# Performance work log

Measured on AMD Instinct MI355X. Metric: run time of the kernel, lower is better.

## Reference

```python
import jax, jax.numpy as jnp
import numpy as np

N_EMBD = 1024
N_HEAD = 16
B, T = 2, 2048
EPS_LN = 1e-5
EPS_RENORM = 1e-8


def _layernorm(x, w, b):
    mu = jnp.mean(x, axis=-1, keepdims=True)
    var = jnp.mean(jnp.square(x - mu), axis=-1, keepdims=True)
    return (x - mu) * jax.lax.rsqrt(var + EPS_LN) * w + b


def setup_inputs() -> dict:
    key = jax.random.key(0)
    ks = jax.random.split(key, 8)
    C = N_EMBD
    s = 0.02
    return {
        "x": jax.random.normal(ks[0], (B, T, C), jnp.float32),
        "ln1_w": jnp.ones((C,), jnp.float32),
        "ln1_b": jnp.zeros((C,), jnp.float32),
        "w_attn": jax.random.normal(ks[1], (C, 3 * C), jnp.float32) * s,
        "b_attn": jnp.zeros((3 * C,), jnp.float32),
        "w_attn_proj": jax.random.normal(ks[2], (C, C), jnp.float32) * s,
        "b_attn_proj": jnp.zeros((C,), jnp.float32),
        "threshold": jnp.full((N_HEAD,), 0.01, jnp.float32),
        "leak": jnp.full((N_HEAD,), 2.0, jnp.float32),
        "steepness": jnp.full((N_HEAD,), 2.0, jnp.float32),
        "ln2_w": jnp.ones((C,), jnp.float32),
        "ln2_b": jnp.zeros((C,), jnp.float32),
        "w_fc": jax.random.normal(ks[3], (C, 4 * C), jnp.float32) * s,
        "b_fc": jnp.zeros((4 * C,), jnp.float32),
        "w_mlp_proj": jax.random.normal(ks[4], (4 * C, C), jnp.float32) * s,
        "b_mlp_proj": jnp.zeros((C,), jnp.float32),
    }


def _ember_block(x, ln1_w, ln1_b, w_attn, b_attn, w_attn_proj, b_attn_proj,
                 threshold, leak, steepness, ln2_w, ln2_b,
                 w_fc, b_fc, w_mlp_proj, b_mlp_proj):
    Bx, Tx, C = x.shape
    H = N_HEAD
    D = C // H

    h = _layernorm(x, ln1_w, ln1_b)
    qkv = h @ w_attn + b_attn                      # [B,T,3C]
    q, k, v = jnp.split(qkv, 3, axis=-1)
    q = q.reshape(Bx, Tx, H, D).transpose(0, 2, 1, 3)  # [B,H,T,D]
    k = k.reshape(Bx, Tx, H, D).transpose(0, 2, 1, 3)
    v = v.reshape(Bx, Tx, H, D).transpose(0, 2, 1, 3)

    att = jnp.einsum('bhqd,bhkd->bhqk', q, k) * (1.0 / np.sqrt(D))
    causal = jnp.tril(jnp.ones((Tx, Tx), bool))
    att = jnp.where(causal[None, None], att, -jnp.inf)
    p = jax.nn.softmax(att, axis=-1)               # [B,H,T,T]

    # per-head LIF gating
    th = (jnp.abs(threshold) * 0.1)[None, :, None, None]
    lk = jax.nn.sigmoid(leak)[None, :, None, None]
    st = jax.nn.softplus(steepness)[None, :, None, None]
    fire = jax.nn.sigmoid(st * (p - th))
    w = fire + lk * (1.0 - fire)
    m = p * w
    m = m / (jnp.sum(m, axis=-1, keepdims=True) + EPS_RENORM)

    y = jnp.einsum('bhqk,bhkd->bhqd', m, v)
    y = y.transpose(0, 2, 1, 3).reshape(Bx, Tx, C)
    y = y @ w_attn_proj + b_attn_proj
    x = x + y

    h2 = _layernorm(x, ln2_w, ln2_b)
    h2 = jax.nn.gelu(h2 @ w_fc + b_fc, approximate=False)
    x = x + (h2 @ w_mlp_proj + b_mlp_proj)
    return x


def reference(x, ln1_w, ln1_b, w_attn, b_attn, w_attn_proj, b_attn_proj,
              threshold, leak, steepness, ln2_w, ln2_b,
              w_fc, b_fc, w_mlp_proj, b_mlp_proj):
    return _ember_block(x, ln1_w, ln1_b, w_attn, b_attn, w_attn_proj, b_attn_proj,
                        threshold, leak, steepness, ln2_w, ln2_b,
                        w_fc, b_fc, w_mlp_proj, b_mlp_proj)
```

## Files before the change

### kernel.cpp

```cpp
#include <hip/hip_runtime.h>
#include <hip/hip_bf16.h>
#include <math.h>

typedef __bf16 bf16_t;
typedef __bf16 bf16x8 __attribute__((ext_vector_type(8)));
typedef __bf16 bf16x4 __attribute__((ext_vector_type(4)));
typedef float  f32x4  __attribute__((ext_vector_type(4)));
typedef unsigned int u32;

static constexpr int C_    = 1024;
static constexpr int NH    = 16;
static constexpr int DH    = 64;
static constexpr int BB    = 2;
static constexpr int TT    = 2048;
static constexpr int MROWS = BB * TT;
static constexpr float LOG2E = 1.4426950408889634f;

__device__ __forceinline__ void gload_lds16(const bf16_t* src, bf16_t* dst) {
  __builtin_amdgcn_global_load_lds(
      (const __attribute__((address_space(1))) u32*)(src),
      (__attribute__((address_space(3))) u32*)(dst),
      16, 0, 0);
}

__device__ __forceinline__ u32 cvt_pk_bf16(float a, float b) {
  u32 r;
  asm("v_cvt_pk_bf16_f32 %0, %1, %2" : "=v"(r) : "v"(a), "v"(b));
  return r;
}

__device__ __forceinline__ float fexp2(float x) {
#if __has_builtin(__builtin_amdgcn_exp2f)
  return __builtin_amdgcn_exp2f(x);
#else
  return exp2f(x);
#endif
}
__device__ __forceinline__ float frcp(float x) {
#if __has_builtin(__builtin_amdgcn_rcpf)
  return __builtin_amdgcn_rcpf(x);
#else
  return 1.0f / x;
#endif
}

__device__ __forceinline__ int sc_to_t(int s, int c) {
  if (s < 32)  return s;
  if (s < 64)  return 32 + (s - 32) * 2 + c;
  if (s < 96)  return 96 + (s - 64) * 3 + c;
  return 192 + (s - 96) * 4 + c;
}

__device__ __forceinline__ void item64_to_uc(int item, int& u, int& c) {
  if (item < 8)       { u = item;               c = 0; }
  else if (item < 24) { int v = item - 8;  u = 8  + (v >> 1); c = v & 1; }
  else if (item < 48) { int v = item - 24; u = 16 + v / 3;    c = v - 3 * (v / 3); }
  else                { int v = item - 48; u = 24 + (v >> 2); c = v & 3; }
}

__global__ __launch_bounds__(256) void ln_bf16(
    const float* __restrict__ x, const float* __restrict__ w,
    const float* __restrict__ b, bf16_t* __restrict__ out)
{
  const int row = blockIdx.x;
  const int tid = threadIdx.x;
  const float4 v = reinterpret_cast<const float4*>(x + (size_t)row * C_)[tid];
  float s  = v.x + v.y + v.z + v.w;
  float s2 = v.x*v.x + v.y*v.y + v.z*v.z + v.w*v.w;
#pragma unroll
  for (int m = 1; m < 64; m <<= 1) { s += __shfl_xor(s, m); s2 += __shfl_xor(s2, m); }
  __shared__ float red[8];
  const int wv = tid >> 6;
  if ((tid & 63) == 0) { red[wv] = s; red[4 + wv] = s2; }
  __syncthreads();
  s  = red[0] + red[1] + red[2] + red[3];
  s2 = red[4] + red[5] + red[6] + red[7];
  const float mu   = s * (1.0f / C_);
  const float rstd = rsqrtf(s2 * (1.0f / C_) - mu * mu + 1e-5f);
  const float4 wv4 = reinterpret_cast<const float4*>(w)[tid];
  const float4 bv4 = reinterpret_cast<const float4*>(b)[tid];
  bf16x4 o;
  o[0] = (bf16_t)((v.x - mu) * rstd * wv4.x + bv4.x);
  o[1] = (bf16_t)((v.y - mu) * rstd * wv4.y + bv4.y);
  o[2] = (bf16_t)((v.z - mu) * rstd * wv4.z + bv4.z);
  o[3] = (bf16_t)((v.w - mu) * rstd * wv4.w + bv4.w);
  *reinterpret_cast<bf16x4*>(out + (size_t)row * C_ + tid * 4) = o;
}

__global__ __launch_bounds__(256) void ln2_fuse(
    const float* __restrict__ p0, const bf16_t* __restrict__ p1,
    const float* __restrict__ xin, const float* __restrict__ pbias,
    const float* __restrict__ w, const float* __restrict__ b,
    float* __restrict__ x2out, bf16_t* __restrict__ out)
{
  const int row = blockIdx.x;
  const int tid = threadIdx.x;
  const size_t base = (size_t)row * C_ + tid * 4;
  const float4 v0 = *reinterpret_cast<const float4*>(p0 + base);
  const bf16x4 v1 = *reinterpret_cast<const bf16x4*>(p1 + base);
  const float4 xr = *reinterpret_cast<const float4*>(xin + base);
  const float4 pb = *reinterpret_cast<const float4*>(pbias + tid * 4);
  float4 v;
  v.x = v0.x + (float)v1[0] + pb.x + xr.x;
  v.y = v0.y + (float)v1[1] + pb.y + xr.y;
  v.z = v0.z + (float)v1[2] + pb.z + xr.z;
  v.w = v0.w + (float)v1[3] + pb.w + xr.w;
  *reinterpret_cast<float4*>(x2out + base) = v;

  float s  = v.x + v.y + v.z + v.w;
  float s2 = v.x*v.x + v.y*v.y + v.z*v.z + v.w*v.w;
#pragma unroll
  for (int m = 1; m < 64; m <<= 1) { s += __shfl_xor(s, m); s2 += __shfl_xor(s2, m); }
  __shared__ float red[8];
  const int wv = tid >> 6;
  if ((tid & 63) == 0) { red[wv] = s; red[4 + wv] = s2; }
  __syncthreads();
  s  = red[0] + red[1] + red[2] + red[3];
  s2 = red[4] + red[5] + red[6] + red[7];
  const float mu   = s * (1.0f / C_);
  const float rstd = rsqrtf(s2 * (1.0f / C_) - mu * mu + 1e-5f);
  const float4 wv4 = reinterpret_cast<const float4*>(w)[tid];
  const float4 bv4 = reinterpret_cast<const float4*>(b)[tid];
  bf16x4 o;
  o[0] = (bf16_t)((v.x - mu) * rstd * wv4.x + bv4.x);
  o[1] = (bf16_t)((v.y - mu) * rstd * wv4.y + bv4.y);
  o[2] = (bf16_t)((v.z - mu) * rstd * wv4.z + bv4.z);
  o[3] = (bf16_t)((v.w - mu) * rstd * wv4.w + bv4.w);
  *reinterpret_cast<bf16x4*>(out + base) = o;
}

__global__ __launch_bounds__(256) void combine3(
    float* __restrict__ out, const bf16_t* __restrict__ p1,
    const bf16_t* __restrict__ p2, const bf16_t* __restrict__ p3,
    const float* __restrict__ bias, const float* __restrict__ resid)
{
  const size_t idx = ((size_t)blockIdx.x * 256 + threadIdx.x) * 4;
  float4 o = *reinterpret_cast<const float4*>(out + idx);
  const bf16x4 a = *reinterpret_cast<const bf16x4*>(p1 + idx);
  const bf16x4 b = *reinterpret_cast<const bf16x4*>(p2 + idx);
  const bf16x4 c = *reinterpret_cast<const bf16x4*>(p3 + idx);
  const float4 r = *reinterpret_cast<const float4*>(resid + idx);
  const int col = (int)(idx & (C_ - 1));
  const float4 bv = *reinterpret_cast<const float4*>(bias + col);
  o.x += (float)a[0] + (float)b[0] + (float)c[0] + bv.x + r.x;
  o.y += (float)a[1] + (float)b[1] + (float)c[1] + bv.y + r.y;
  o.z += (float)a[2] + (float)b[2] + (float)c[2] + bv.z + r.z;
  o.w += (float)a[3] + (float)b[3] + (float)c[3] + bv.w + r.w;
  *reinterpret_cast<float4*>(out + idx) = o;
}

__global__ __launch_bounds__(256) void transpose_w(
    const float* __restrict__ in, bf16_t* __restrict__ out, int K, int N)
{
  __shared__ float tile[32][33];
  const int tx = threadIdx.x & 31, ty = threadIdx.x >> 5;
  const int n0 = blockIdx.x * 32, k0 = blockIdx.y * 32;
#pragma unroll
  for (int i = 0; i < 4; ++i)
    tile[ty + i * 8][tx] = in[(size_t)(k0 + ty + i * 8) * N + n0 + tx];
  __syncthreads();
#pragma unroll
  for (int i = 0; i < 4; ++i)
    out[(size_t)(n0 + ty + i * 8) * K + k0 + tx] = (bf16_t)tile[tx][ty + i * 8];
}

__global__ __launch_bounds__(256) void transpose_v(
    const bf16_t* __restrict__ in, bf16_t* __restrict__ out)
{
  __shared__ bf16_t tile[32][33];
  const int bh = blockIdx.z;
  const bf16_t* src = in  + (size_t)bh * TT * DH;
  bf16_t*       dst = out + (size_t)bh * TT * DH;
  const int tx = threadIdx.x & 31, ty = threadIdx.x >> 5;
  const int t0 = blockIdx.x * 32, d0 = blockIdx.y * 32;
#pragma unroll
  for (int i = 0; i < 4; ++i)
    tile[ty + i * 8][tx] = src[(size_t)(t0 + ty + i * 8) * DH + d0 + tx];
  __syncthreads();
#pragma unroll
  for (int i = 0; i < 4; ++i)
    dst[(size_t)(d0 + ty + i * 8) * TT + t0 + tx] = tile[tx][ty + i * 8];
}

template<int EPI>
__global__ __launch_bounds__(512, 2) void gemm256(
    const bf16_t* __restrict__ A, const bf16_t* __restrict__ Bt,
    const float* __restrict__ bias, bf16_t* __restrict__ bout0,
    bf16_t* __restrict__ bout1, bf16_t* __restrict__ bout2,
    int N, int K, int nbn)
{
  __shared__ bf16_t As[2][256 * 64];
  __shared__ bf16_t Bs[2][256 * 64];
  const int tid  = threadIdx.x;
  const int wave = tid >> 6, lane = tid & 63;
  const int r = lane & 15, g = lane >> 4;
  const int wm = wave >> 2, wn = wave & 3;

  const int cpx = gridDim.x >> 3;
  const int swz = (blockIdx.x & 7) * cpx + (blockIdx.x >> 3);
  const int bm = swz / nbn, bn = swz - bm * nbn;

  const bf16_t* Abase = A  + (size_t)bm * 256 * K;
  const bf16_t* Bbase = Bt + (size_t)bn * 256 * K;

  f32x4 acc[8][4] = {};

  auto STAGE = [&](int b, int kt) {
#pragma unroll
    for (int it = 0; it < 4; ++it) {
      const int idx = it * 512 + tid;
      const int rr = idx >> 3, cc = idx & 7, gs = cc ^ (rr & 7);
      gload_lds16(Abase + (size_t)rr * K + kt + gs * 8, &As[b][idx * 8]);
      gload_lds16(Bbase + (size_t)rr * K + kt + gs * 8, &Bs[b][idx * 8]);
    }
  };

  const int NT = K >> 6;
  STAGE(0, 0);
  for (int t = 0; t < NT; ++t) {
    const int b = t & 1;
    if (t + 1 < NT) {
      STAGE(b ^ 1, (t + 1) << 6);
      asm volatile("s_waitcnt vmcnt(8)" ::: "memory");
    } else {
      asm volatile("s_waitcnt vmcnt(0)" ::: "memory");
    }
    __builtin_amdgcn_s_barrier();
    asm volatile("" ::: "memory");
#pragma unroll
    for (int s2 = 0; s2 < 2; ++s2) {
      bf16x8 af[8], bfr[4];
#pragma unroll
      for (int mi = 0; mi < 8; ++mi) {
        const int rr = wm * 128 + mi * 16 + r;
        const int ch = (s2 * 4 + g) ^ (rr & 7);
        af[mi] = *reinterpret_cast<const bf16x8*>(&As[b][rr * 64 + ch * 8]);
      }
#pragma unroll
      for (int ni = 0; ni < 4; ++ni) {
        const int rr = wn * 64 + ni * 16 + r;
        const int ch = (s2 * 4 + g) ^ (rr & 7);
        bfr[ni] = *reinterpret_cast<const bf16x8*>(&Bs[b][rr * 64 + ch * 8]);
      }
      __builtin_amdgcn_s_setprio(1);
#pragma unroll
      for (int mi = 0; mi < 8; ++mi)
#pragma unroll
        for (int ni = 0; ni < 4; ++ni)
          acc[mi][ni] = __builtin_amdgcn_mfma_f32_16x16x32_bf16(
              af[mi], bfr[ni], acc[mi][ni], 0, 0, 0);
      __builtin_amdgcn_s_setprio(0);
    }
    asm volatile("" ::: "memory");
    __builtin_amdgcn_s_barrier();
  }

#pragma unroll
  for (int mi = 0; mi < 8; ++mi) {
#pragma unroll
    for (int ni = 0; ni < 4; ++ni) {
      const int grow0 = bm * 256 + wm * 128 + mi * 16 + g * 4;
      const int gcol  = bn * 256 + wn * 64 + ni * 16 + r;
      const float bv = bias[gcol];
#pragma unroll
      for (int i = 0; i < 4; ++i) {
        const int grow = grow0 + i;
        const float v = acc[mi][ni][i] + bv;
        if constexpr (EPI == 0) {
          const int which = gcol >> 10;
          const int c0 = gcol & 1023;
          const int hh = c0 >> 6, dd = c0 & 63;
          const int bb = grow >> 11, tt = grow & 2047;
          bf16_t* dst = (which == 0) ? bout0 : (which == 1) ? bout1 : bout2;
          dst[((size_t)(bb * NH + hh) * TT + tt) * DH + dd] = (bf16_t)v;
        } else {
          const float gl = 0.5f * v * (1.0f + erff(v * 0.70710678118654752f));
          bout0[(size_t)grow * N + gcol] = (bf16_t)gl;
        }
      }
    }
  }
}

template<int EPI>
__global__ __launch_bounds__(256) void gemm_bf16(
    const bf16_t* __restrict__ A, const bf16_t* __restrict__ Bt,
    const float* __restrict__ bias, const float* __restrict__ resid,
    float* __restrict__ fout, bf16_t* __restrict__ bout0,
    bf16_t* __restrict__ bout1, bf16_t* __restrict__ bout2,
    int M, int N, int Kc, int Kfull)
{
  constexpr int BM = 128, BN = 128, BK = 64;
  __shared__ bf16_t As[BM * BK];
  __shared__ bf16_t Bs[BN * BK];
  const int tid  = threadIdx.x;
  const int wave = tid >> 6, lane = tid & 63;
  const int r = lane & 15, g = lane >> 4;
  const int wm = wave >> 1, wn = wave & 1;
  const int bm = blockIdx.x, bn = blockIdx.y;
  const int z  = blockIdx.z;
  const int kstart = z * Kc;

  const bf16_t* Abase = A  + (size_t)bm * BM * Kfull;
  const bf16_t* Bbase = Bt + (size_t)bn * BN * Kfull;

  f32x4 acc[4][4] = {};

  for (int kt = kstart; kt < kstart + Kc; kt += BK) {
#pragma unroll
    for (int it = 0; it < 4; ++it) {
      const int c0 = it * 256 + wave * 64;
      const int idx = c0 + lane;
      const int rr = idx >> 3, cc = idx & 7;
      const int gs = cc ^ (rr & 7);
      gload_lds16(Abase + (size_t)rr * Kfull + kt + gs * 8, As + c0 * 8);
    }
#pragma unroll
    for (int it = 0; it < 4; ++it) {
      const int c0 = it * 256 + wave * 64;
      const int idx = c0 + lane;
      const int rr = idx >> 3, cc = idx & 7;
      const int gs = cc ^ (rr & 7);
      gload_lds16(Bbase + (size_t)rr * Kfull + kt + gs * 8, Bs + c0 * 8);
    }
    asm volatile("s_waitcnt vmcnt(0)" ::: "memory");
    __syncthreads();
#pragma unroll
    for (int s = 0; s < 2; ++s) {
      bf16x8 af[4], bfr[4];
#pragma unroll
      for (int mi = 0; mi < 4; ++mi) {
        const int rr = wm * 64 + mi * 16 + r;
        const int ch = (s * 4 + g) ^ (rr & 7);
        af[mi] = *reinterpret_cast<const bf16x8*>(&As[rr * BK + ch * 8]);
      }
#pragma unroll
      for (int ni = 0; ni < 4; ++ni) {
        const int rr = wn * 64 + ni * 16 + r;
        const int ch = (s * 4 + g) ^ (rr & 7);
        bfr[ni] = *reinterpret_cast<const bf16x8*>(&Bs[rr * BK + ch * 8]);
      }
#pragma unroll
      for (int mi = 0; mi < 4; ++mi)
#pragma unroll
        for (int ni = 0; ni < 4; ++ni)
          acc[mi][ni] = __builtin_amdgcn_mfma_f32_16x16x32_bf16(
              af[mi], bfr[ni], acc[mi][ni], 0, 0, 0);
    }
    __syncthreads();
  }

#pragma unroll
  for (int mi = 0; mi < 4; ++mi) {
#pragma unroll
    for (int ni = 0; ni < 4; ++ni) {
      const int grow0 = bm * BM + wm * 64 + mi * 16 + g * 4;
      const int gcol  = bn * BN + wn * 64 + ni * 16 + r;
#pragma unroll
      for (int i = 0; i < 4; ++i) {
        const int grow = grow0 + i;
        const float v = acc[mi][ni][i];
        const size_t o = (size_t)grow * N + gcol;
        if (z == 0) fout[o] = v;
        else {
          bf16_t* pb = (z == 1) ? bout0 : (z == 2) ? bout1 : bout2;
          pb[o] = (bf16_t)v;
        }
      }
    }
  }
}


__global__ __launch_bounds__(256, 4) void attn_p1(
    const bf16_t* __restrict__ Q, const bf16_t* __restrict__ Km,
    float2* __restrict__ mzP)
{
  __shared__ bf16_t Ks[2][64 * 64];
  const int tid = threadIdx.x;
  const int w = tid >> 6, lane = tid & 63;
  const int r = lane & 15, g = lane >> 4;
  const int bid = blockIdx.x;
  const int bh  = (bid & 7) * 4 + ((bid >> 3) & 3);
  int u, c; item64_to_uc(bid >> 5, u, c);
  const int cmax = u >> 3;
  const bool diag = (c == cmax);
  const int nt = diag ? (u & 7) + 1 : 8;
  const int s = 4 * u + w;
  const int row0 = u * 64 + w * 16;
  const int qrow = row0 + r;

  const bf16_t* Qh = Q  + (size_t)bh * TT * DH;
  const bf16_t* Kh = Km + (size_t)bh * TT * DH;
  const float SCL = 0.125f * LOG2E;

  bf16x8 qf[2];
#pragma unroll
  for (int s2 = 0; s2 < 2; ++s2) {
    bf16x8 t = *reinterpret_cast<const bf16x8*>(Qh + (size_t)qrow * DH + s2 * 32 + g * 8);
#pragma unroll
    for (int i = 0; i < 8; ++i) t[i] = (bf16_t)((float)t[i] * SCL);
    qf[s2] = t;
  }

  auto STAGEK = [&](int b, int t8) {
#pragma unroll
    for (int it = 0; it < 2; ++it) {
      const int idx = it * 256 + tid;
      const int rr = idx >> 3, cc = idx & 7, gs = cc ^ (rr & 7);
      gload_lds16(Kh + (size_t)(c * 512 + t8 * 64 + rr) * DH + gs * 8, &Ks[b][idx * 8]);
    }
  };

  float runM = -1e30f, runZ = 0.f;
  STAGEK(0, 0);
  for (int t8 = 0; t8 < nt; ++t8) {
    const int b = t8 & 1;
    asm volatile("s_waitcnt vmcnt(0)" ::: "memory");
    __syncthreads();
    if (t8 + 1 < nt) STAGEK(b ^ 1, t8 + 1);
    f32x4 sfT[4] = {};
#pragma unroll
    for (int s2 = 0; s2 < 2; ++s2) {
      bf16x8 kf[4];
#pragma unroll
      for (int ni = 0; ni < 4; ++ni)
        kf[ni] = *reinterpret_cast<const bf16x8*>(
            &Ks[b][(ni * 16 + r) * 64 + (((s2 << 2) | g) ^ (r & 7)) * 8]);
#pragma unroll
      for (int ni = 0; ni < 4; ++ni)
        sfT[ni] = __builtin_amdgcn_mfma_f32_16x16x32_bf16(kf[ni], qf[s2], sfT[ni], 0, 0, 0);
    }
    const bool dm = diag && (t8 == nt - 1);
    const int kbase = c * 512 + t8 * 64;
    float xv[16];
#pragma unroll
    for (int ni = 0; ni < 4; ++ni)
#pragma unroll
      for (int j = 0; j < 4; ++j) {
        float x = sfT[ni][j];
        if (dm) {
          const int kcol = kbase + ni * 16 + g * 4 + j;
          if (kcol > qrow) x = -1e30f;
        }
        xv[ni * 4 + j] = x;
      }
    float nm = runM;
#pragma unroll
    for (int e = 0; e < 16; ++e) nm = fmaxf(nm, xv[e]);
    float z = runZ * fexp2(runM - nm);
#pragma unroll
    for (int e = 0; e < 16; ++e) z += fexp2(xv[e] - nm);
    runM = nm; runZ = z;
  }
#pragma unroll
  for (int msk = 16; msk < 64; msk <<= 1) {
    const float om = __shfl_xor(runM, msk), oz = __shfl_xor(runZ, msk);
    const float nm = fmaxf(runM, om);
    runZ = runZ * fexp2(runM - nm) + oz * fexp2(om - nm);
    runM = nm;
  }
  if (lane < 16)
    mzP[((size_t)(bh * 128 + s) * 4 + c) * 16 + r] = make_float2(runM, runZ);
}

__global__ __launch_bounds__(256, 4) void attn_p3(
    const bf16_t* __restrict__ Q, const bf16_t* __restrict__ Km,
    const bf16_t* __restrict__ Vt, const float2* __restrict__ mzP,
    bf16_t* __restrict__ Y, uint2* __restrict__ yaccA,
    uint2* __restrict__ yaccB, float* __restrict__ denP,
    const float* __restrict__ thrp, const float* __restrict__ leakp,
    const float* __restrict__ steepp)
{
  __shared__ bf16_t Ks[2][64 * 64];
  __shared__ bf16_t Vs[2][64 * 64];
  __shared__ __align__(16) u32 Ms[4][512];

  const int tid = threadIdx.x;
  const int w = tid >> 6, lane = tid & 63;
  const int r = lane & 15, g = lane >> 4;
  const int bid = blockIdx.x;
  const int bh  = (bid & 7) * 4 + ((bid >> 3) & 3);
  int u, c; item64_to_uc(bid >> 5, u, c);
  const int cmax = u >> 3;
  const bool diag = (c == cmax);
  const int nt = diag ? (u & 7) + 1 : 8;
  const int nch = cmax + 1;
  const int s = 4 * u + w;
  const int row0 = u * 64 + w * 16;
  const int qrow = row0 + r;
  const int hh = bh & (NH - 1), bb = bh >> 4;

  const bf16_t* Qh  = Q  + (size_t)bh * TT * DH;
  const bf16_t* Kh  = Km + (size_t)bh * TT * DH;
  const bf16_t* Vth = Vt + (size_t)bh * TT * DH;

  const float lk  = 1.0f / (1.0f + expf(-leakp[hh]));
  const float ilk = 1.0f - lk;
  const float st  = log1pf(expf(steepp[hh]));
  const float Lst = LOG2E * st;
  const float A0  = Lst * (fabsf(thrp[hh]) * 0.1f);

  float M = -1e30f, Z = 0.f;
  for (int c2 = 0; c2 < nch; ++c2) {
    const float2 mz = mzP[((size_t)(bh * 128 + s) * 4 + c2) * 16 + r];
    const float nm = fmaxf(M, mz.x);
    Z = Z * fexp2(M - nm) + mz.y * fexp2(mz.x - nm);
    M = nm;
  }
  const float rcpZ = frcp(Z);

  const float SCL = 0.125f * LOG2E;
  bf16x8 qf[2];
#pragma unroll
  for (int s2 = 0; s2 < 2; ++s2) {
    bf16x8 t = *reinterpret_cast<const bf16x8*>(Qh + (size_t)qrow * DH + s2 * 32 + g * 8);
#pragma unroll
    for (int i = 0; i < 8; ++i) t[i] = (bf16_t)((float)t[i] * SCL);
    qf[s2] = t;
  }
  bf16x8 ones;
#pragma unroll
  for (int i = 0; i < 8; ++i) ones[i] = (bf16_t)1.0f;

  uint2* MsU2 = reinterpret_cast<uint2*>(&Ms[w][0]);
  uint4* MsU4 = reinterpret_cast<uint4*>(&Ms[w][0]);

  auto STAGE = [&](int b, int t8) {
    const int kbase = c * 512 + t8 * 64;
#pragma unroll
    for (int it = 0; it < 2; ++it) {
      const int idx = it * 256 + tid;
      const int rr = idx >> 3, cc = idx & 7, gs = cc ^ (rr & 7);
      gload_lds16(Kh + (size_t)(kbase + rr) * DH + gs * 8, &Ks[b][idx * 8]);
      gload_lds16(Vth + (size_t)rr * TT + kbase + gs * 8, &Vs[b][idx * 8]);
    }
  };

  f32x4 yacc[4] = {};
  f32x4 dacc = {};

  STAGE(0, 0);
  for (int t8 = 0; t8 < nt; ++t8) {
    const int b = t8 & 1;
    asm volatile("s_waitcnt vmcnt(0)" ::: "memory");
    __syncthreads();
    if (t8 + 1 < nt) STAGE(b ^ 1, t8 + 1);
    const int kbase = c * 512 + t8 * 64;
    f32x4 sfT[4] = {};
#pragma unroll
    for (int s2 = 0; s2 < 2; ++s2) {
      bf16x8 kf[4];
#pragma unroll
      for (int ni = 0; ni < 4; ++ni)
        kf[ni] = *reinterpret_cast<const bf16x8*>(
            &Ks[b][(ni * 16 + r) * 64 + (((s2 << 2) | g) ^ (r & 7)) * 8]);
#pragma unroll
      for (int ni = 0; ni < 4; ++ni)
        sfT[ni] = __builtin_amdgcn_mfma_f32_16x16x32_bf16(kf[ni], qf[s2], sfT[ni], 0, 0, 0);
    }
    const bool dm = diag && (t8 == nt - 1);
#pragma unroll
    for (int ni = 0; ni < 4; ++ni) {
      float mv[4];
#pragma unroll
      for (int j = 0; j < 4; ++j) {
        float x = sfT[ni][j];
        if (dm) {
          const int kcol = kbase + ni * 16 + g * 4 + j;
          if (kcol > qrow) x = -1e30f;
        }
        const float p    = fexp2(x - M) * rcpZ;
        const float fire = frcp(1.0f + fexp2(A0 - Lst * p));
        mv[j] = p * fmaf(ilk, fire, lk);
      }
      MsU2[r * 16 + ((4 * ni + g) ^ ((r & 7) << 1))] =
          make_uint2(cvt_pk_bf16(mv[0], mv[1]), cvt_pk_bf16(mv[2], mv[3]));
    }
#pragma unroll
    for (int s2 = 0; s2 < 2; ++s2) {
      const uint4 aw = MsU4[r * 8 + ((s2 * 4 + g) ^ (r & 7))];
      const bf16x8 af = __builtin_bit_cast(bf16x8, aw);
      bf16x8 vf[4];
#pragma unroll
      for (int ni = 0; ni < 4; ++ni)
        vf[ni] = *reinterpret_cast<const bf16x8*>(
            &Vs[b][(ni * 16 + r) * 64 + (((s2 << 2) | g) ^ (r & 7)) * 8]);
#pragma unroll
      for (int ni = 0; ni < 4; ++ni)
        yacc[ni] = __builtin_amdgcn_mfma_f32_16x16x32_bf16(af, vf[ni], yacc[ni], 0, 0, 0);
      dacc = __builtin_amdgcn_mfma_f32_16x16x32_bf16(af, ones, dacc, 0, 0, 0);
    }
  }

  if (nch == 1) {
#pragma unroll
    for (int j = 0; j < 4; ++j) {
      const float rd = frcp(dacc[j] + 1e-8f);
      const int t = row0 + g * 4 + j;
#pragma unroll
      for (int ni = 0; ni < 4; ++ni)
        Y[((size_t)(bb * TT + t)) * C_ + hh * DH + ni * 16 + r] =
            (bf16_t)(yacc[ni][j] * rd);
    }
  } else {
    const int pid = bh * 288 + (sc_to_t(s, c) - 32);
    uint2* pb = (pid < 4096) ? (yaccA + (size_t)pid * 256)
                             : (yaccB + (size_t)(pid - 4096) * 256);
#pragma unroll
    for (int ni = 0; ni < 4; ++ni)
      pb[ni * 64 + lane] =
          make_uint2(cvt_pk_bf16(yacc[ni][0], yacc[ni][1]),
                     cvt_pk_bf16(yacc[ni][2], yacc[ni][3]));
    if (r == 0)
      *reinterpret_cast<float4*>(&denP[(size_t)pid * 16 + g * 4]) =
          make_float4(dacc[0], dacc[1], dacc[2], dacc[3]);
  }
}

__global__ __launch_bounds__(256) void attn_p4(
    const uint2* __restrict__ yaccA, const uint2* __restrict__ yaccB,
    const float* __restrict__ denP, bf16_t* __restrict__ Y)
{
  const int bid = blockIdx.x;
  const int bh  = bid / 96;
  const int s   = 32 + (bid - bh * 96);
  const int nch = (s >> 5) + 1;
  const int hh = bh & (NH - 1), bb = bh >> 4;

  const int tid = threadIdx.x;
  const int w = tid >> 6, lane = tid & 63;
  const int r = lane & 15, g = lane >> 4;

  float acc[4] = {};
  float den[4] = {};
  for (int c = 0; c < nch; ++c) {
    const int pid = bh * 288 + (sc_to_t(s, c) - 32);
    const uint2* pb = (pid < 4096) ? (yaccA + (size_t)pid * 256)
                                   : (yaccB + (size_t)(pid - 4096) * 256);
    const uint2 u = pb[w * 64 + lane];
    acc[0] += __builtin_bit_cast(float, (u.x & 0xFFFFu) << 16);
    acc[1] += __builtin_bit_cast(float, (u.x & 0xFFFF0000u));
    acc[2] += __builtin_bit_cast(float, (u.y & 0xFFFFu) << 16);
    acc[3] += __builtin_bit_cast(float, (u.y & 0xFFFF0000u));
    const float4 d4 = *reinterpret_cast<const float4*>(&denP[(size_t)pid * 16 + g * 4]);
    den[0] += d4.x; den[1] += d4.y; den[2] += d4.z; den[3] += d4.w;
  }
#pragma unroll
  for (int j = 0; j < 4; ++j) {
    const float rd = 1.0f / (den[j] + 1e-8f);
    const int t = s * 16 + g * 4 + j;
    Y[((size_t)(bb * TT + t)) * C_ + hh * DH + w * 16 + r] = (bf16_t)(acc[j] * rd);
  }
}

extern "C" void kernel_launch(void* const* d_in, const int* in_sizes, int n_in,
                              void* d_out, int out_size, void* d_ws, size_t ws_size,
                              hipStream_t stream)
{
  const float* x      = (const float*)d_in[0];
  const float* ln1_w  = (const float*)d_in[1];
  const float* ln1_b  = (const float*)d_in[2];
  const float* w_attn = (const float*)d_in[3];
  const float* b_attn = (const float*)d_in[4];
  const float* w_proj = (const float*)d_in[5];
  const float* b_proj = (const float*)d_in[6];
  const float* thr    = (const float*)d_in[7];
  const float* leak   = (const float*)d_in[8];
  const float* steep  = (const float*)d_in[9];
  const float* ln2_w  = (const float*)d_in[10];
  const float* ln2_b  = (const float*)d_in[11];
  const float* w_fc   = (const float*)d_in[12];
  const float* b_fc   = (const float*)d_in[13];
  const float* w_mlp  = (const float*)d_in[14];
  const float* b_mlp  = (const float*)d_in[15];

  char* ws = (char*)d_ws;
  bf16_t* q    = (bf16_t*)(ws + 0);
  bf16_t* k    = (bf16_t*)(ws + 8388608);
  bf16_t* v    = (bf16_t*)(ws + 16777216);
  bf16_t* vT   = (bf16_t*)(ws + 25165824);
  bf16_t* gbuf = (bf16_t*)(ws + 0);
  bf16_t* hbuf = (bf16_t*)(ws + 33554432);
  float*  x2   = (float*) (ws + 41943040);
  bf16_t* wT_attn = (bf16_t*)(ws + 58720256);
  bf16_t* wT_proj = (bf16_t*)(ws + 65011712);
  bf16_t* wT_fc   = (bf16_t*)(ws + 67108864);
  bf16_t* wT_mlp  = (bf16_t*)(ws + 75497472);

  uint2* yaccA = (uint2*)(ws + 16777216);
  uint2* yaccB = (uint2*)(ws + 41943040);
  float* denP  = (float*)(ws + 52428800);
  float2* mzP  = (float2*)(ws + 53477376);

  bf16_t* pp1 = (bf16_t*)(ws + 0);
  bf16_t* mp1 = (bf16_t*)(ws + 33554432);
  bf16_t* mp2 = (bf16_t*)(ws + 58720256);
  bf16_t* mp3 = (bf16_t*)(ws + 67108864);

  float* out = (float*)d_out;

  ln_bf16<<<dim3(MROWS), dim3(256), 0, stream>>>(x, ln1_w, ln1_b, hbuf);
  transpose_w<<<dim3(96, 32),  dim3(256), 0, stream>>>(w_attn, wT_attn, 1024, 3072);
  transpose_w<<<dim3(32, 32),  dim3(256), 0, stream>>>(w_proj, wT_proj, 1024, 1024);
  transpose_w<<<dim3(128, 32), dim3(256), 0, stream>>>(w_fc,   wT_fc,   1024, 4096);
  transpose_w<<<dim3(32, 128), dim3(256), 0, stream>>>(w_mlp,  wT_mlp,  4096, 1024);

  gemm256<0><<<dim3(192), dim3(512), 0, stream>>>(
      hbuf, wT_attn, b_attn, q, k, v, 3072, 1024, 12);
  transpose_v<<<dim3(64, 2, 32), dim3(256), 0, stream>>>(v, vT);

  attn_p1<<<dim3(2560), dim3(256), 0, stream>>>(q, k, mzP);
  attn_p3<<<dim3(2560), dim3(256), 0, stream>>>(
      q, k, vT, mzP, hbuf, yaccA, yaccB, denP, thr, leak, steep);
  attn_p4<<<dim3(3072), dim3(256), 0, stream>>>(yaccA, yaccB, denP, hbuf);

  gemm_bf16<3><<<dim3(32, 8, 2), dim3(256), 0, stream>>>(
      hbuf, wT_proj, nullptr, nullptr, x2, pp1, nullptr, nullptr,
      MROWS, 1024, 512, 1024);

  ln2_fuse<<<dim3(MROWS), dim3(256), 0, stream>>>(
      x2, pp1, x, b_proj, ln2_w, ln2_b, x2, hbuf);

  gemm256<2><<<dim3(256), dim3(512), 0, stream>>>(
      hbuf, wT_fc, b_fc, gbuf, nullptr, nullptr, 4096, 1024, 16);

  gemm_bf16<3><<<dim3(32, 8, 4), dim3(256), 0, stream>>>(
      gbuf, wT_mlp, nullptr, nullptr, out, mp1, mp2, mp3,
      MROWS, 1024, 1024, 4096);

  combine3<<<dim3(4096), dim3(256), 0, stream>>>(out, mp1, mp2, mp3, b_mlp, x2);
}
```

Measured before the change: 295.5 us.

## Interleave next-tile global loads with MFMA phases in GEMM main loop

Restructures the 256x256 GEMM main loop into four phases per K-tile, each loading a quarter of the A fragments and issuing half of the next tile's global-to-LDS prefetch during the first two phases. Barriers are placed around each phase so the memory traffic is spread across the MFMA work instead of being issued all at once. Fewer A fragments are live at a time, which reduces register pressure. The cost is more barriers per K-tile and a full vmcnt(0) wait at the end of each tile.

New measurement: 291.3 us. Within noise of the previous version (-1.4%).

```diff
diff --git a/kernel.cpp b/kernel.cpp
--- a/kernel.cpp
+++ b/kernel.cpp
@@ -205,9 +205,9 @@
 
   f32x4 acc[8][4] = {};
 
-  auto STAGE = [&](int b, int kt) {
-#pragma unroll
-    for (int it = 0; it < 4; ++it) {
+  auto STAGE2 = [&](int b, int kt, int half) {
+#pragma unroll
+    for (int it = half * 2; it < half * 2 + 2; ++it) {
       const int idx = it * 512 + tid;
       const int rr = idx >> 3, cc = idx & 7, gs = cc ^ (rr & 7);
       gload_lds16(Abase + (size_t)rr * K + kt + gs * 8, &As[b][idx * 8]);
@@ -216,43 +216,48 @@
   };
 
   const int NT = K >> 6;
-  STAGE(0, 0);
+  STAGE2(0, 0, 0); STAGE2(0, 0, 1);
+  asm volatile("s_waitcnt vmcnt(0)" ::: "memory");
+  __builtin_amdgcn_s_barrier();
+
   for (int t = 0; t < NT; ++t) {
     const int b = t & 1;
-    if (t + 1 < NT) {
-      STAGE(b ^ 1, (t + 1) << 6);
-      asm volatile("s_waitcnt vmcnt(8)" ::: "memory");
-    } else {
-      asm volatile("s_waitcnt vmcnt(0)" ::: "memory");
-    }
-    __builtin_amdgcn_s_barrier();
-    asm volatile("" ::: "memory");
-#pragma unroll
-    for (int s2 = 0; s2 < 2; ++s2) {
-      bf16x8 af[8], bfr[4];
-#pragma unroll
-      for (int mi = 0; mi < 8; ++mi) {
-        const int rr = wm * 128 + mi * 16 + r;
+    const bool pre = (t + 1 < NT);
+    const int kn = (t + 1) << 6;
+    bf16x8 bfr[4];
+#pragma unroll
+    for (int p = 0; p < 4; ++p) {
+      const int s2 = p >> 1, mh = p & 1;
+      if (mh == 0) {
+#pragma unroll
+        for (int ni = 0; ni < 4; ++ni) {
+          const int rr = wn * 64 + ni * 16 + r;
+          const int ch = (s2 * 4 + g) ^ (rr & 7);
+          bfr[ni] = *reinterpret_cast<const bf16x8*>(&Bs[b][rr * 64 + ch * 8]);
+        }
+      }
+      bf16x8 af[4];
+#pragma unroll
+      for (int mi = 0; mi < 4; ++mi) {
+        const int rr = wm * 128 + (mh * 4 + mi) * 16 + r;
         const int ch = (s2 * 4 + g) ^ (rr & 7);
         af[mi] = *reinterpret_cast<const bf16x8*>(&As[b][rr * 64 + ch * 8]);
       }
-#pragma unroll
-      for (int ni = 0; ni < 4; ++ni) {
-        const int rr = wn * 64 + ni * 16 + r;
-        const int ch = (s2 * 4 + g) ^ (rr & 7);
-        bfr[ni] = *reinterpret_cast<const bf16x8*>(&Bs[b][rr * 64 + ch * 8]);
-      }
+      if (pre && p < 2) STAGE2(b ^ 1, kn, p);
+      __builtin_amdgcn_s_barrier();
       __builtin_amdgcn_s_setprio(1);
 #pragma unroll
-      for (int mi = 0; mi < 8; ++mi)
+      for (int mi = 0; mi < 4; ++mi)
 #pragma unroll
         for (int ni = 0; ni < 4; ++ni)
-          acc[mi][ni] = __builtin_amdgcn_mfma_f32_16x16x32_bf16(
-              af[mi], bfr[ni], acc[mi][ni], 0, 0, 0);
+          acc[mh * 4 + mi][ni] = __builtin_amdgcn_mfma_f32_16x16x32_bf16(
+              af[mi], bfr[ni], acc[mh * 4 + mi][ni], 0, 0, 0);
       __builtin_amdgcn_s_setprio(0);
-    }
-    asm volatile("" ::: "memory");
-    __builtin_amdgcn_s_barrier();
+      __builtin_amdgcn_sched_barrier(0);
+      if (p == 3)
+        asm volatile("s_waitcnt vmcnt(0)" ::: "memory");
+      __builtin_amdgcn_s_barrier();
+    }
   }
 
 #pragma unroll
```
